# Optimization experiments

Hardware: AMD Instinct MI355X
Metric: run time of the kernel (lower is better)

## Reference

```python
import jax, jax.numpy as jnp
import numpy as np

H = 16      # num_heads
HD = 128    # head_dim
P = 5       # num_paths
STAT = 4
HIDDEN = 2048
GATE_IN = HIDDEN + H * STAT * P + H * P + H * (P * (P - 1) // 2)  # 2608
GATE_HID = HIDDEN // 2  # 1024
OUT_DIM = H * P


def setup_inputs() -> dict:
    key = jax.random.key(0)
    ks = jax.random.split(key, 10)
    B, L = 2, 4096
    inp = {"hidden_states": jax.random.normal(ks[0], (B, L, HIDDEN), jnp.float32)}
    for i in range(P):
        inp[f"p{i}"] = jax.random.normal(ks[1 + i], (B, L, H, HD), jnp.float32)
    # QuantizedLinear treated as standard Linear (torch default init)
    s1 = 1.0 / np.sqrt(GATE_IN)
    s2 = 1.0 / np.sqrt(GATE_HID)
    inp["W1"] = jax.random.uniform(ks[6], (GATE_HID, GATE_IN), jnp.float32, -s1, s1)
    inp["b1"] = jax.random.uniform(ks[7], (GATE_HID,), jnp.float32, -s1, s1)
    inp["W2"] = jax.random.uniform(ks[8], (OUT_DIM, GATE_HID), jnp.float32, -s2, s2)
    # bias init: zero then favor paths 3 (value) and 4 (identity)
    b2 = np.zeros((H, P), np.float32)
    b2[:, 3] = 1.0
    b2[:, 4] = 2.0
    inp["b2"] = jnp.asarray(b2.reshape(-1))
    inp["log_temp"] = jnp.zeros((H, 1), jnp.float32)  # log(temp_init=1.0)
    return inp


def _forward(hidden_states, paths, W1, b1, W2, b2, log_temp):
    B, L, _ = hidden_states.shape
    ps = jnp.stack(paths, axis=-1)  # [B,L,H,D,P]
    # --- per-path stats over head_dim ---
    mean = ps.mean(axis=-2)                      # [B,L,H,P]
    var = ps.var(axis=-2)                        # unbiased=False
    abs_mean = jnp.abs(ps).mean(axis=-2)
    sq = jnp.sum(ps * ps, axis=-2)               # [B,L,H,P]
    l2 = jnp.sqrt(sq)
    stats = jnp.stack([mean, var, abs_mean, l2], axis=-1)   # [B,L,H,P,STAT] -> (p s) order
    stats_flat = stats.reshape(B, L, H, P * STAT)
    norms_flat = l2                                         # [B,L,H,P]
    # --- pairwise L2 distances: ||a-b||^2 = ||a||^2+||b||^2-2<a,b> ---
    dots = jnp.einsum('blhdp,blhdq->blhpq', ps, ps)
    d2 = sq[..., :, None] + sq[..., None, :] - 2.0 * dots
    dist = jnp.sqrt(jnp.clip(d2, 0.0, None))                # [B,L,H,P,P]
    iu0, iu1 = np.triu_indices(P, k=1)
    pairwise = dist[..., iu0, iu1]                           # [B,L,H,P*(P-1)/2]
    # --- router MLP ---
    gate_input = jnp.concatenate([
        hidden_states,
        stats_flat.reshape(B, L, -1),
        norms_flat.reshape(B, L, -1),
        pairwise.reshape(B, L, -1),
    ], axis=-1)  # [B,L,GATE_IN]
    h = jax.nn.gelu(gate_input @ W1.T + b1, approximate=False)
    logits = (h @ W2.T + b2).reshape(B, L, H, P)
    temp = jnp.exp(log_temp)[None, None]                     # [1,1,H,1]
    probs = jax.nn.softmax(logits / temp, axis=-1)
    probs = jnp.clip(probs, 0.02, None)
    probs = probs / probs.sum(axis=-1, keepdims=True)
    output = jnp.einsum('blhdp,blhp->blhd', ps, probs)       # [B,L,H,HD]
    return output


def reference(hidden_states, p0, p1, p2, p3, p4, W1, b1, W2, b2, log_temp):
    out = _forward(hidden_states, [p0, p1, p2, p3, p4], W1, b1, W2, b2, log_temp)
    reg_loss = jnp.float32(0.0)  # eval mode: no entropy regularizer
    return out, reg_loss
```

## Files before the change

### kernel.cpp

```cpp
#include <hip/hip_runtime.h>
#include <hip/hip_bf16.h>
#include <cstdint>
#include <cstddef>

typedef _Float16 half8 __attribute__((ext_vector_type(8)));
typedef _Float16 half4 __attribute__((ext_vector_type(4)));
typedef _Float16 half2v __attribute__((ext_vector_type(2)));
typedef float floatx4 __attribute__((ext_vector_type(4)));

#define KIN   2608
#define KP    2624
#define GH    1024
#define NOUT  80
#define NTOK  8192
#define HID   2048

__device__ __forceinline__ void async_copy16(const void* gsrc, void* ldst) {
  __builtin_amdgcn_global_load_lds(
      (const __attribute__((address_space(1))) void*)gsrc,
      (__attribute__((address_space(3))) void*)ldst, 16, 0, 0);
}

__global__ __launch_bounds__(256) void convertw(
    const float* __restrict__ W1, const float* __restrict__ W2,
    _Float16* __restrict__ W1p, _Float16* __restrict__ W2p)
{
  int i = blockIdx.x * 256 + threadIdx.x;
  const int total1 = GH * KP;
  if (i < total1) {
    int n = i / KP;
    int k = i - n * KP;
    W1p[i] = (k < KIN) ? (_Float16)W1[(size_t)n * KIN + k] : (_Float16)0.f;
  } else {
    int j = i - total1;
    if (j < NOUT * GH) W2p[j] = (_Float16)W2[j];
  }
}

__global__ __launch_bounds__(256) void convh(
    const float* __restrict__ hidden, _Float16* __restrict__ gate)
{
  int i = blockIdx.x * 256 + threadIdx.x;
  int token = i >> 8;
  int c = i & 255;
  const float4* src = (const float4*)(hidden + (size_t)token * HID + c * 8);
  float4 a = src[0], b = src[1];
  half8 hv;
  hv[0] = (_Float16)a.x; hv[1] = (_Float16)a.y; hv[2] = (_Float16)a.z; hv[3] = (_Float16)a.w;
  hv[4] = (_Float16)b.x; hv[5] = (_Float16)b.y; hv[6] = (_Float16)b.z; hv[7] = (_Float16)b.w;
  *(half8*)(gate + (size_t)token * KP + c * 8) = hv;
}

__global__ __launch_bounds__(256) void k1_stats(
    const float* __restrict__ p0, const float* __restrict__ p1,
    const float* __restrict__ p2, const float* __restrict__ p3,
    const float* __restrict__ p4,
    _Float16* __restrict__ gate)
{
  const int gid = blockIdx.x * 256 + threadIdx.x;
  const int token = gid >> 4;
  const int h = gid & 15;
  const size_t base = (size_t)gid * 128;
  const float* paths[5] = {p0, p1, p2, p3, p4};

  float s[5], s2[5], sa[5], dt[10];
#pragma unroll
  for (int p = 0; p < 5; ++p) { s[p] = 0.f; s2[p] = 0.f; sa[p] = 0.f; }
#pragma unroll
  for (int i = 0; i < 10; ++i) dt[i] = 0.f;

#pragma unroll 2
  for (int c = 0; c < 16; ++c) {
    float v[5][8];
#pragma unroll
    for (int p = 0; p < 5; ++p) {
      const float4* q = (const float4*)(paths[p] + base + c * 8);
      float4 x0 = q[0], x1 = q[1];
      v[p][0] = x0.x; v[p][1] = x0.y; v[p][2] = x0.z; v[p][3] = x0.w;
      v[p][4] = x1.x; v[p][5] = x1.y; v[p][6] = x1.z; v[p][7] = x1.w;
    }
#pragma unroll
    for (int p = 0; p < 5; ++p) {
#pragma unroll
      for (int e = 0; e < 8; ++e) {
        float x = v[p][e];
        s[p] += x; s2[p] += x * x; sa[p] += fabsf(x);
      }
    }
    int pi = 0;
#pragma unroll
    for (int a = 0; a < 5; ++a)
#pragma unroll
      for (int b = a + 1; b < 5; ++b) {
        float d = 0.f;
#pragma unroll
        for (int e = 0; e < 8; ++e) d += v[a][e] * v[b][e];
        dt[pi++] += d;
      }
  }

  _Float16* gs = gate + (size_t)token * KP;
  float l2v[5];
#pragma unroll
  for (int p = 0; p < 5; ++p) {
    float mean = s[p] * (1.f / 128.f);
    float var  = s2[p] * (1.f / 128.f) - mean * mean;
    float am   = sa[p] * (1.f / 128.f);
    float l2   = sqrtf(s2[p]);
    l2v[p] = l2;
    half4 st;
    st[0] = (_Float16)mean; st[1] = (_Float16)var;
    st[2] = (_Float16)am;   st[3] = (_Float16)l2;
    *(half4*)(gs + 2048 + h * 20 + p * 4) = st;
  }
#pragma unroll
  for (int p = 0; p < 5; ++p) gs[2368 + h * 5 + p] = (_Float16)l2v[p];
  {
    float pw[10];
    int pi = 0;
#pragma unroll
    for (int a = 0; a < 5; ++a)
#pragma unroll
      for (int b = a + 1; b < 5; ++b) {
        float d2 = s2[a] + s2[b] - 2.f * dt[pi];
        pw[pi] = sqrtf(fmaxf(d2, 0.f));
        ++pi;
      }
#pragma unroll
    for (int i = 0; i < 5; ++i) {
      half2v t; t[0] = (_Float16)pw[2 * i]; t[1] = (_Float16)pw[2 * i + 1];
      *(half2v*)(gs + 2448 + h * 10 + 2 * i) = t;
    }
  }
  if (h == 0) {
    half8 z = {(_Float16)0.f, (_Float16)0.f, (_Float16)0.f, (_Float16)0.f,
               (_Float16)0.f, (_Float16)0.f, (_Float16)0.f, (_Float16)0.f};
    *(half8*)(gs + 2608) = z;
    *(half8*)(gs + 2616) = z;
  }
}

__global__ __launch_bounds__(256) void gemm1(
    const _Float16* __restrict__ A,
    const _Float16* __restrict__ Bt,
    const float* __restrict__ b1,
    _Float16* __restrict__ Hm)
{
  __shared__ _Float16 As[128 * 64];
  __shared__ _Float16 Bs[128 * 64];
  const int tid  = threadIdx.x;
  const int lane = tid & 63;
  const int wave = tid >> 6;
  const int m0 = blockIdx.x * 128;
  const int n0 = blockIdx.y * 128;
  const int wm = (wave & 1) * 64;
  const int wn = (wave >> 1) * 64;

  floatx4 acc[4][4];
#pragma unroll
  for (int i = 0; i < 4; ++i)
#pragma unroll
    for (int k = 0; k < 4; ++k) acc[i][k] = (floatx4){0.f, 0.f, 0.f, 0.f};

  for (int kt = 0; kt < KP / 64; ++kt) {
    __syncthreads();
    const int kbase = kt * 64;
#pragma unroll
    for (int r = 0; r < 4; ++r) {
      int chunk = r * 256 + tid;
      int row = chunk >> 3;
      int kk  = (chunk & 7) * 8;
      const _Float16* ga = A  + (size_t)(m0 + row) * KP + kbase + kk;
      const _Float16* gb = Bt + (size_t)(n0 + row) * KP + kbase + kk;
      async_copy16(ga, &As[0] + (r * 2048 + wave * 512));
      async_copy16(gb, &Bs[0] + (r * 2048 + wave * 512));
    }
    __syncthreads();
#pragma unroll
    for (int ks = 0; ks < 2; ++ks) {
      half8 af[4], bf[4];
#pragma unroll
      for (int i = 0; i < 4; ++i) {
        int ar = wm + i * 16 + (lane & 15);
        af[i] = *(const half8*)&As[ar * 64 + ks * 32 + (lane >> 4) * 8];
        int br = wn + i * 16 + (lane & 15);
        bf[i] = *(const half8*)&Bs[br * 64 + ks * 32 + (lane >> 4) * 8];
      }
#pragma unroll
      for (int mi = 0; mi < 4; ++mi)
#pragma unroll
        for (int ni = 0; ni < 4; ++ni)
          acc[mi][ni] = __builtin_amdgcn_mfma_f32_16x16x32_f16(af[mi], bf[ni], acc[mi][ni], 0, 0, 0);
    }
  }
#pragma unroll
  for (int mi = 0; mi < 4; ++mi) {
#pragma unroll
    for (int ni = 0; ni < 4; ++ni) {
      int col = n0 + wn + ni * 16 + (lane & 15);
      float bias = b1[col];
#pragma unroll
      for (int r = 0; r < 4; ++r) {
        int row = m0 + wm + mi * 16 + (lane >> 4) * 4 + r;
        float x = acc[mi][ni][r] + bias;
        float g = 0.5f * x * (1.f + erff(x * 0.70710678118654752f));
        Hm[(size_t)row * GH + col] = (_Float16)g;
      }
    }
  }
}

__global__ __launch_bounds__(256) void gemm2(
    const _Float16* __restrict__ Hm, const _Float16* __restrict__ W2p,
    const float* __restrict__ b2, float* __restrict__ logits)
{
  const int lane = threadIdx.x & 63;
  const int wave = threadIdx.x >> 6;
  const int m0 = blockIdx.x * 64 + wave * 16;
  const int mrow = m0 + (lane & 15);
  const int koff = (lane >> 4) * 8;
  floatx4 acc[5];
#pragma unroll
  for (int i = 0; i < 5; ++i) acc[i] = (floatx4){0.f, 0.f, 0.f, 0.f};
  for (int k0 = 0; k0 < GH; k0 += 32) {
    half8 af = *(const half8*)&Hm[(size_t)mrow * GH + k0 + koff];
#pragma unroll
    for (int ni = 0; ni < 5; ++ni) {
      half8 bf = *(const half8*)&W2p[(size_t)(ni * 16 + (lane & 15)) * GH + k0 + koff];
      acc[ni] = __builtin_amdgcn_mfma_f32_16x16x32_f16(af, bf, acc[ni], 0, 0, 0);
    }
  }
#pragma unroll
  for (int ni = 0; ni < 5; ++ni) {
    int col = ni * 16 + (lane & 15);
    float bias = b2[col];
#pragma unroll
    for (int r = 0; r < 4; ++r) {
      int row = m0 + (lane >> 4) * 4 + r;
      logits[(size_t)row * NOUT + col] = acc[ni][r] + bias;
    }
  }
}

__global__ __launch_bounds__(256) void softmaxk(
    const float* __restrict__ logits, const float* __restrict__ log_temp,
    float* __restrict__ probs)
{
  int id = blockIdx.x * 256 + threadIdx.x;
  int t = id >> 4;
  int h = id & 15;
  float it = __expf(-log_temp[h]);
  const float* lp = logits + (size_t)t * NOUT + h * 5;
  float x[5];
  float m = -1e30f;
#pragma unroll
  for (int p = 0; p < 5; ++p) { x[p] = lp[p] * it; m = fmaxf(m, x[p]); }
  float ssum = 0.f;
#pragma unroll
  for (int p = 0; p < 5; ++p) { x[p] = __expf(x[p] - m); ssum += x[p]; }
  float inv = 1.f / ssum;
  float c = 0.f;
#pragma unroll
  for (int p = 0; p < 5; ++p) { x[p] = fmaxf(x[p] * inv, 0.02f); c += x[p]; }
  float inv2 = 1.f / c;
  float* pp = probs + (size_t)t * NOUT + h * 5;
#pragma unroll
  for (int p = 0; p < 5; ++p) pp[p] = x[p] * inv2;
}

__global__ __launch_bounds__(256) void k5_combine(
    const float* __restrict__ p0, const float* __restrict__ p1,
    const float* __restrict__ p2, const float* __restrict__ p3,
    const float* __restrict__ p4,
    const float* __restrict__ probs, float* __restrict__ out)
{
  size_t i4 = (size_t)blockIdx.x * 256 + threadIdx.x;
  int token = (int)(i4 >> 9);
  int rem = (int)(i4 & 511);
  int h = rem >> 5;
  const float* pb = probs + (size_t)token * NOUT + h * 5;
  float w0 = pb[0], w1 = pb[1], w2 = pb[2], w3 = pb[3], w4 = pb[4];
  size_t off = i4 * 4;
  float4 a0 = *(const float4*)(p0 + off);
  float4 a1 = *(const float4*)(p1 + off);
  float4 a2 = *(const float4*)(p2 + off);
  float4 a3 = *(const float4*)(p3 + off);
  float4 a4 = *(const float4*)(p4 + off);
  float4 r;
  r.x = a0.x * w0 + a1.x * w1 + a2.x * w2 + a3.x * w3 + a4.x * w4;
  r.y = a0.y * w0 + a1.y * w1 + a2.y * w2 + a3.y * w3 + a4.y * w4;
  r.z = a0.z * w0 + a1.z * w1 + a2.z * w2 + a3.z * w3 + a4.z * w4;
  r.w = a0.w * w0 + a1.w * w1 + a2.w * w2 + a3.w * w3 + a4.w * w4;
  *(float4*)(out + off) = r;
  if (i4 == 0) out[(size_t)NTOK * 2048] = 0.f;
}

extern "C" void kernel_launch(void* const* d_in, const int* in_sizes, int n_in,
                              void* d_out, int out_size, void* d_ws, size_t ws_size,
                              hipStream_t stream) {
  const float* hidden  = (const float*)d_in[0];
  const float* p0      = (const float*)d_in[1];
  const float* p1      = (const float*)d_in[2];
  const float* p2      = (const float*)d_in[3];
  const float* p3      = (const float*)d_in[4];
  const float* p4      = (const float*)d_in[5];
  const float* W1      = (const float*)d_in[6];
  const float* b1      = (const float*)d_in[7];
  const float* W2      = (const float*)d_in[8];
  const float* b2      = (const float*)d_in[9];
  const float* logtemp = (const float*)d_in[10];
  float* out = (float*)d_out;

  char* ws = (char*)d_ws;
  _Float16* gate = (_Float16*)(ws);
  _Float16* W1p  = (_Float16*)(ws + 42991616);
  _Float16* W2p  = (_Float16*)(ws + 48365568);
  _Float16* Hm   = (_Float16*)(ws + 48529408);
  float*    logits = (float*)(ws + 65306624);
  float*    probs  = (float*)(ws + 67928064);

  convertw<<<10816, 256, 0, stream>>>(W1, W2, W1p, W2p);
  convh<<<8192, 256, 0, stream>>>(hidden, gate);
  k1_stats<<<512, 256, 0, stream>>>(p0, p1, p2, p3, p4, gate);
  gemm1<<<dim3(NTOK / 128, GH / 128), 256, 0, stream>>>(gate, W1p, b1, Hm);
  gemm2<<<NTOK / 64, 256, 0, stream>>>(Hm, W2p, b2, logits);
  softmaxk<<<(NTOK * 16) / 256, 256, 0, stream>>>(logits, logtemp, probs);
  k5_combine<<<(NTOK * 2048 / 4) / 256, 256, 0, stream>>>(p0, p1, p2, p3, p4, probs, out);
}
```

Baseline: 607.6 us.

## Fuse hidden-state conversion into stats kernel and split head reduction across four lanes

Merges the hidden-state fp32→fp16 conversion kernel into the path-statistics kernel, so one launch writes the whole gate row. The stats work is remapped so four lanes share one head, each reading interleaved float4 chunks, with the partial sums combined by shuffles. The output writes are also split across those lanes. This aims to cut one launch, raise the number of blocks from 512 to 2048 for better parallelism, and give coalesced loads instead of strided 32-byte per-thread reads. The cost is extra shuffle instructions and divergent write branches.

```diff
diff --git a/kernel.cpp b/kernel.cpp
--- a/kernel.cpp
+++ b/kernel.cpp
@@ -37,31 +37,20 @@
   }
 }
 
-__global__ __launch_bounds__(256) void convh(
-    const float* __restrict__ hidden, _Float16* __restrict__ gate)
-{
-  int i = blockIdx.x * 256 + threadIdx.x;
-  int token = i >> 8;
-  int c = i & 255;
-  const float4* src = (const float4*)(hidden + (size_t)token * HID + c * 8);
-  float4 a = src[0], b = src[1];
-  half8 hv;
-  hv[0] = (_Float16)a.x; hv[1] = (_Float16)a.y; hv[2] = (_Float16)a.z; hv[3] = (_Float16)a.w;
-  hv[4] = (_Float16)b.x; hv[5] = (_Float16)b.y; hv[6] = (_Float16)b.z; hv[7] = (_Float16)b.w;
-  *(half8*)(gate + (size_t)token * KP + c * 8) = hv;
-}
-
-__global__ __launch_bounds__(256) void k1_stats(
+__global__ __launch_bounds__(256) void k1_fused(
+    const float* __restrict__ hidden,
     const float* __restrict__ p0, const float* __restrict__ p1,
     const float* __restrict__ p2, const float* __restrict__ p3,
     const float* __restrict__ p4,
     _Float16* __restrict__ gate)
 {
-  const int gid = blockIdx.x * 256 + threadIdx.x;
-  const int token = gid >> 4;
-  const int h = gid & 15;
-  const size_t base = (size_t)gid * 128;
+  const int wave = threadIdx.x >> 6;
+  const int lane = threadIdx.x & 63;
+  const int token = blockIdx.x * 4 + wave;
+  const int h = lane >> 2;
+  const int sub = lane & 3;
   const float* paths[5] = {p0, p1, p2, p3, p4};
+  const size_t hb = ((size_t)token * 16 + h) * 128;
 
   float s[5], s2[5], sa[5], dt[10];
 #pragma unroll
@@ -69,20 +58,19 @@
 #pragma unroll
   for (int i = 0; i < 10; ++i) dt[i] = 0.f;
 
-#pragma unroll 2
-  for (int c = 0; c < 16; ++c) {
-    float v[5][8];
+#pragma unroll
+  for (int j = 0; j < 8; ++j) {
+    const int chunk = sub + j * 4;
+    float v[5][4];
 #pragma unroll
     for (int p = 0; p < 5; ++p) {
-      const float4* q = (const float4*)(paths[p] + base + c * 8);
-      float4 x0 = q[0], x1 = q[1];
-      v[p][0] = x0.x; v[p][1] = x0.y; v[p][2] = x0.z; v[p][3] = x0.w;
-      v[p][4] = x1.x; v[p][5] = x1.y; v[p][6] = x1.z; v[p][7] = x1.w;
+      float4 x = *(const float4*)(paths[p] + hb + chunk * 4);
+      v[p][0] = x.x; v[p][1] = x.y; v[p][2] = x.z; v[p][3] = x.w;
     }
 #pragma unroll
     for (int p = 0; p < 5; ++p) {
 #pragma unroll
-      for (int e = 0; e < 8; ++e) {
+      for (int e = 0; e < 4; ++e) {
         float x = v[p][e];
         s[p] += x; s2[p] += x * x; sa[p] += fabsf(x);
       }
@@ -94,28 +82,51 @@
       for (int b = a + 1; b < 5; ++b) {
         float d = 0.f;
 #pragma unroll
-        for (int e = 0; e < 8; ++e) d += v[a][e] * v[b][e];
+        for (int e = 0; e < 4; ++e) d += v[a][e] * v[b][e];
         dt[pi++] += d;
       }
   }
 
+#pragma unroll
+  for (int p = 0; p < 5; ++p) {
+    s[p]  += __shfl_xor(s[p], 1, 4);  s[p]  += __shfl_xor(s[p], 2, 4);
+    s2[p] += __shfl_xor(s2[p], 1, 4); s2[p] += __shfl_xor(s2[p], 2, 4);
+    sa[p] += __shfl_xor(sa[p], 1, 4); sa[p] += __shfl_xor(sa[p], 2, 4);
+  }
+#pragma unroll
+  for (int i = 0; i < 10; ++i) {
+    dt[i] += __shfl_xor(dt[i], 1, 4); dt[i] += __shfl_xor(dt[i], 2, 4);
+  }
+
   _Float16* gs = gate + (size_t)token * KP;
-  float l2v[5];
-#pragma unroll
-  for (int p = 0; p < 5; ++p) {
-    float mean = s[p] * (1.f / 128.f);
-    float var  = s2[p] * (1.f / 128.f) - mean * mean;
-    float am   = sa[p] * (1.f / 128.f);
-    float l2   = sqrtf(s2[p]);
-    l2v[p] = l2;
-    half4 st;
-    st[0] = (_Float16)mean; st[1] = (_Float16)var;
-    st[2] = (_Float16)am;   st[3] = (_Float16)l2;
-    *(half4*)(gs + 2048 + h * 20 + p * 4) = st;
-  }
-#pragma unroll
-  for (int p = 0; p < 5; ++p) gs[2368 + h * 5 + p] = (_Float16)l2v[p];
-  {
+  if (sub < 2) {
+#pragma unroll
+    for (int q = 0; q < 2; ++q) {
+      int p = sub * 2 + q;
+      float mean = s[p] * (1.f / 128.f);
+      float var  = s2[p] * (1.f / 128.f) - mean * mean;
+      float am   = sa[p] * (1.f / 128.f);
+      float l2   = sqrtf(s2[p]);
+      half4 st;
+      st[0] = (_Float16)mean; st[1] = (_Float16)var;
+      st[2] = (_Float16)am;   st[3] = (_Float16)l2;
+      *(half4*)(gs + 2048 + h * 20 + p * 4) = st;
+    }
+  } else if (sub == 2) {
+    {
+      int p = 4;
+      float mean = s[p] * (1.f / 128.f);
+      float var  = s2[p] * (1.f / 128.f) - mean * mean;
+      float am   = sa[p] * (1.f / 128.f);
+      float l2   = sqrtf(s2[p]);
+      half4 st;
+      st[0] = (_Float16)mean; st[1] = (_Float16)var;
+      st[2] = (_Float16)am;   st[3] = (_Float16)l2;
+      *(half4*)(gs + 2048 + h * 20 + p * 4) = st;
+    }
+#pragma unroll
+    for (int p = 0; p < 5; ++p) gs[2368 + h * 5 + p] = (_Float16)sqrtf(s2[p]);
+  } else {
     float pw[10];
     int pi = 0;
 #pragma unroll
@@ -131,12 +142,24 @@
       half2v t; t[0] = (_Float16)pw[2 * i]; t[1] = (_Float16)pw[2 * i + 1];
       *(half2v*)(gs + 2448 + h * 10 + 2 * i) = t;
     }
-  }
-  if (h == 0) {
-    half8 z = {(_Float16)0.f, (_Float16)0.f, (_Float16)0.f, (_Float16)0.f,
-               (_Float16)0.f, (_Float16)0.f, (_Float16)0.f, (_Float16)0.f};
-    *(half8*)(gs + 2608) = z;
-    *(half8*)(gs + 2616) = z;
+    if (h == 0) {
+      half8 z = {(_Float16)0.f, (_Float16)0.f, (_Float16)0.f, (_Float16)0.f,
+                 (_Float16)0.f, (_Float16)0.f, (_Float16)0.f, (_Float16)0.f};
+      *(half8*)(gs + 2608) = z;
+      *(half8*)(gs + 2616) = z;
+    }
+  }
+
+  const float* hrow = hidden + (size_t)token * HID;
+#pragma unroll
+  for (int j = 0; j < 4; ++j) {
+    int c = lane + 64 * j;
+    float4 a = *(const float4*)(hrow + c * 8);
+    float4 b = *(const float4*)(hrow + c * 8 + 4);
+    half8 hv;
+    hv[0] = (_Float16)a.x; hv[1] = (_Float16)a.y; hv[2] = (_Float16)a.z; hv[3] = (_Float16)a.w;
+    hv[4] = (_Float16)b.x; hv[5] = (_Float16)b.y; hv[6] = (_Float16)b.z; hv[7] = (_Float16)b.w;
+    *(half8*)(gs + c * 8) = hv;
   }
 }
 
@@ -320,8 +343,7 @@
   float*    probs  = (float*)(ws + 67928064);
 
   convertw<<<10816, 256, 0, stream>>>(W1, W2, W1p, W2p);
-  convh<<<8192, 256, 0, stream>>>(hidden, gate);
-  k1_stats<<<512, 256, 0, stream>>>(p0, p1, p2, p3, p4, gate);
+  k1_fused<<<2048, 256, 0, stream>>>(hidden, p0, p1, p2, p3, p4, gate);
   gemm1<<<dim3(NTOK / 128, GH / 128), 256, 0, stream>>>(gate, W1p, b1, Hm);
   gemm2<<<NTOK / 64, 256, 0, stream>>>(Hm, W2p, b2, logits);
   softmaxk<<<(NTOK * 16) / 256, 256, 0, stream>>>(logits, logtemp, probs);
```

After: 564.4 us. 1.08x faster.
